# Performance work log

Hardware: AMD Instinct MI355X
Metric: run time of the kernel (lower is better)

The kernel has to match this reference:

```python
import jax, jax.numpy as jnp
import numpy as np

DIM = 768
HEADS = 12
DIM_HEAD = 64
INNER = HEADS * DIM_HEAD  # 768
EPS = 1e-5


def setup_inputs() -> dict:
    key = jax.random.key(0)
    ks = jax.random.split(key, 5)
    x = jax.random.normal(ks[0], (4, 2048, DIM), dtype=jnp.float32)
    ln_g = jnp.ones((DIM,), dtype=jnp.float32)
    ln_b = jnp.zeros((DIM,), dtype=jnp.float32)
    s1 = 1.0 / np.sqrt(DIM)
    W_qkv = jax.random.uniform(ks[1], (DIM, 3 * INNER), dtype=jnp.float32, minval=-s1, maxval=s1)
    b_qkv = jax.random.uniform(ks[2], (3 * INNER,), dtype=jnp.float32, minval=-s1, maxval=s1)
    s2 = 1.0 / np.sqrt(INNER)
    W_out = jax.random.uniform(ks[3], (INNER, DIM), dtype=jnp.float32, minval=-s2, maxval=s2)
    b_out = jax.random.uniform(ks[4], (DIM,), dtype=jnp.float32, minval=-s2, maxval=s2)
    return {"x": x, "ln_g": ln_g, "ln_b": ln_b, "W_qkv": W_qkv, "b_qkv": b_qkv, "W_out": W_out, "b_out": b_out}


def reference(x, ln_g, ln_b, W_qkv, b_qkv, W_out, b_out):
    b, n, _ = x.shape
    # pre-norm LayerNorm
    mu = jnp.mean(x, axis=-1, keepdims=True)
    var = jnp.mean(jnp.square(x - mu), axis=-1, keepdims=True)
    xn = (x - mu) * jax.lax.rsqrt(var + EPS) * ln_g + ln_b
    qkv = xn @ W_qkv + b_qkv  # [b, n, 3*inner]
    q, k, v = jnp.split(qkv, 3, axis=-1)
    def to_heads(t):
        return t.reshape(b, n, HEADS, DIM_HEAD).transpose(0, 2, 1, 3)  # b h n d
    q, k, v = map(to_heads, (q, k, v))
    q = q * (DIM_HEAD ** -0.5)
    sim = jnp.einsum('bhid,bhjd->bhij', q, k)
    attn = jax.nn.softmax(sim, axis=-1)  # dropout is identity (p=0.0)
    out = jnp.einsum('bhij,bhjd->bhid', attn, v)
    out = out.transpose(0, 2, 1, 3).reshape(b, n, INNER)
    return out @ W_out + b_out
```

## Files before the change

### kernel.cpp

```cpp
#include <hip/hip_runtime.h>
#include <cstdint>
#include <cstddef>


#define SEQ    2048
#define NBATCH 4
#define DMODEL 768
#define NHEADS 12
#define DHEAD  64
#define MROWS  (NBATCH * SEQ)
#define NQKV   (3 * DMODEL)
#define KT     64
#define NT     (SEQ / KT)

using f32x4  = __attribute__((ext_vector_type(4))) float;
using u16x8  = __attribute__((ext_vector_type(8))) unsigned short;
using s16x8  = __attribute__((ext_vector_type(8))) short;

__device__ __forceinline__ unsigned short f2bf(float f) {
  union { float f; unsigned int u; } x; x.f = f;
  unsigned int r = x.u + 0x7fffu + ((x.u >> 16) & 1u);
  return (unsigned short)(r >> 16);
}

#if defined(__has_builtin)
#if __has_builtin(__builtin_amdgcn_cvt_pk_bf16_f32)
#define HAVE_PK_BF16 1
#endif
#if __has_builtin(__builtin_amdgcn_exp2f)
#define HAVE_EXP2 1
#endif
#endif

__device__ __forceinline__ unsigned int pk_bf16(float a, float b) {
#ifdef HAVE_PK_BF16
  auto v = __builtin_amdgcn_cvt_pk_bf16_f32(a, b);
  union { decltype(v) v2; unsigned int u; } c; c.v2 = v; return c.u;
#else
  return (unsigned int)f2bf(a) | ((unsigned int)f2bf(b) << 16);
#endif
}

__device__ __forceinline__ float fexp2(float x) {
#ifdef HAVE_EXP2
  return __builtin_amdgcn_exp2f(x);
#else
  return exp2f(x);
#endif
}

__device__ __forceinline__ f32x4 mfma16(u16x8 a, u16x8 b, f32x4 c) {
  return __builtin_amdgcn_mfma_f32_16x16x32_bf16((s16x8)a, (s16x8)b, c, 0, 0, 0);
}

__device__ __forceinline__ void gl_lds16(const void* g, void* l) {
  __builtin_amdgcn_global_load_lds(
      (const __attribute__((address_space(1))) void*)g,
      (__attribute__((address_space(3))) void*)l, 16, 0, 0);
}

__global__ __launch_bounds__(256) void ln_kernel(
    const float* __restrict__ x, const float* __restrict__ g,
    const float* __restrict__ bb, unsigned short* __restrict__ xn) {
  __shared__ float red[8];
  const int row = blockIdx.x, t = threadIdx.x;
  const float* xr = x + (size_t)row * DMODEL;
  float v0 = xr[t], v1 = xr[t + 256], v2 = xr[t + 512];
  float s = v0 + v1 + v2;
#pragma unroll
  for (int o = 32; o; o >>= 1) s += __shfl_down(s, o);
  if ((t & 63) == 0) red[t >> 6] = s;
  __syncthreads();
  float mu = (red[0] + red[1] + red[2] + red[3]) * (1.0f / DMODEL);
  float d0 = v0 - mu, d1 = v1 - mu, d2 = v2 - mu;
  float q = d0 * d0 + d1 * d1 + d2 * d2;
#pragma unroll
  for (int o = 32; o; o >>= 1) q += __shfl_down(q, o);
  if ((t & 63) == 0) red[4 + (t >> 6)] = q;
  __syncthreads();
  float var = (red[4] + red[5] + red[6] + red[7]) * (1.0f / DMODEL);
  float rstd = rsqrtf(var + 1e-5f);
  size_t base = (size_t)row * DMODEL;
  xn[base + t]       = f2bf(d0 * rstd * g[t]       + bb[t]);
  xn[base + t + 256] = f2bf(d1 * rstd * g[t + 256] + bb[t + 256]);
  xn[base + t + 512] = f2bf(d2 * rstd * g[t + 512] + bb[t + 512]);
}

__global__ __launch_bounds__(256) void tconv_kernel(
    const float* __restrict__ W, unsigned short* __restrict__ Wt, int N) {
  __shared__ float tile[32][33];
  const int n0 = blockIdx.x * 32, k0 = blockIdx.y * 32;
  const int tx = threadIdx.x & 31, ty = threadIdx.x >> 5;
#pragma unroll
  for (int r = 0; r < 4; ++r)
    tile[ty + r * 8][tx] = W[(size_t)(k0 + ty + r * 8) * N + n0 + tx];
  __syncthreads();
#pragma unroll
  for (int r = 0; r < 4; ++r)
    Wt[(size_t)(n0 + ty + r * 8) * DMODEL + k0 + tx] = f2bf(tile[tx][ty + r * 8]);
}

__global__ __launch_bounds__(256, 2) void gemm_qk_kernel(
    const unsigned short* __restrict__ Wt, const unsigned short* __restrict__ xn,
    const float* __restrict__ bias, unsigned short* __restrict__ qb,
    unsigned short* __restrict__ kb) {
  __shared__ alignas(16) unsigned short As[128 * 64];
  __shared__ alignas(16) unsigned short Bs[128 * 64];
  const int t = threadIdx.x, wid = t >> 6, l = t & 63, quad = l >> 4, ll = l & 15;
  const int a0 = blockIdx.x * 128;
  const int b0 = blockIdx.y * 128;
  const int wa = (wid >> 1) * 64, wb = (wid & 1) * 64;
  const int srow = l >> 3, sblk = (l & 7) ^ srow;
  f32x4 acc[4][4] = {};
  for (int k0 = 0; k0 < DMODEL; k0 += 64) {
#pragma unroll
    for (int cc = 0; cc < 4; ++cc) {
      int call = wid * 4 + cc;
      int r = call * 8 + srow;
      gl_lds16(Wt + (size_t)(a0 + r) * DMODEL + k0 + sblk * 8, &As[call * 512]);
      gl_lds16(xn + (size_t)(b0 + r) * DMODEL + k0 + sblk * 8, &Bs[call * 512]);
    }
    __syncthreads();
#pragma unroll
    for (int ks = 0; ks < 2; ++ks) {
      u16x8 af[4], bf[4];
#pragma unroll
      for (int i = 0; i < 4; ++i) {
        int ra = wa + i * 16 + ll, rb = wb + i * 16 + ll;
        int blk = (ks * 4 + quad) ^ (ll & 7);
        af[i] = *(const u16x8*)&As[ra * 64 + blk * 8];
        bf[i] = *(const u16x8*)&Bs[rb * 64 + blk * 8];
      }
#pragma unroll
      for (int mi = 0; mi < 4; ++mi)
#pragma unroll
        for (int ni = 0; ni < 4; ++ni)
          acc[mi][ni] = mfma16(af[mi], bf[ni], acc[mi][ni]);
    }
    __syncthreads();
  }
  const bool isq = (a0 < DMODEL);
  unsigned short* dst = isq ? qb : kb;
  const float sc = isq ? 0.18033688f : 1.0f;
#pragma unroll
  for (int mi = 0; mi < 4; ++mi) {
    int row0 = a0 + wa + mi * 16 + quad * 4;
    float4 bv = *(const float4*)&bias[row0];
    int rr = isq ? row0 : row0 - DMODEL;
    int h = rr >> 6, d0 = rr & 63;
#pragma unroll
    for (int ni = 0; ni < 4; ++ni) {
      int seq = b0 + wb + ni * 16 + ll;
      int b = seq >> 11, i = seq & 2047;
      uint2 pk;
      pk.x = pk_bf16((acc[mi][ni][0] + bv.x) * sc, (acc[mi][ni][1] + bv.y) * sc);
      pk.y = pk_bf16((acc[mi][ni][2] + bv.z) * sc, (acc[mi][ni][3] + bv.w) * sc);
      *(uint2*)&dst[(size_t)((b * NHEADS + h) * SEQ + i) * DHEAD + d0] = pk;
    }
  }
}

__global__ __launch_bounds__(256, 2) void gemm_v_kernel(
    const unsigned short* __restrict__ A, const unsigned short* __restrict__ Bt,
    const float* __restrict__ bias, unsigned short* __restrict__ vt) {
  __shared__ alignas(16) unsigned short As[128 * 64];
  __shared__ alignas(16) unsigned short Bs[128 * 64];
  const int t = threadIdx.x, wid = t >> 6, l = t & 63, quad = l >> 4, ll = l & 15;
  const int m0 = blockIdx.x * 128;
  const int n0 = 2 * DMODEL + blockIdx.y * 128;
  const int wm = (wid >> 1) * 64, wn = (wid & 1) * 64;
  const int srow = l >> 3, sblk = (l & 7) ^ srow;
  f32x4 acc[4][4] = {};
  for (int k0 = 0; k0 < DMODEL; k0 += 64) {
#pragma unroll
    for (int cc = 0; cc < 4; ++cc) {
      int call = wid * 4 + cc;
      int r = call * 8 + srow;
      gl_lds16(A  + (size_t)(m0 + r) * DMODEL + k0 + sblk * 8, &As[call * 512]);
      gl_lds16(Bt + (size_t)(n0 + r) * DMODEL + k0 + sblk * 8, &Bs[call * 512]);
    }
    __syncthreads();
#pragma unroll
    for (int ks = 0; ks < 2; ++ks) {
      u16x8 af[4], bf[4];
#pragma unroll
      for (int i = 0; i < 4; ++i) {
        int ra = wm + i * 16 + ll, rb = wn + i * 16 + ll;
        int blk = (ks * 4 + quad) ^ (ll & 7);
        af[i] = *(const u16x8*)&As[ra * 64 + blk * 8];
        bf[i] = *(const u16x8*)&Bs[rb * 64 + blk * 8];
      }
#pragma unroll
      for (int mi = 0; mi < 4; ++mi)
#pragma unroll
        for (int ni = 0; ni < 4; ++ni)
          acc[mi][ni] = mfma16(af[mi], bf[ni], acc[mi][ni]);
    }
    __syncthreads();
  }
#pragma unroll
  for (int mi = 0; mi < 4; ++mi) {
    int gm = m0 + wm + mi * 16 + quad * 4;
    int b = gm >> 11, i0 = gm & 2047;
#pragma unroll
    for (int ni = 0; ni < 4; ++ni) {
      int gn = n0 + wn + ni * 16 + ll;
      float bv = bias[gn];
      int rem = gn - 2 * DMODEL;
      int h = rem >> 6, d = rem & 63;
      int bh = b * NHEADS + h;
      uint2 pk;
      pk.x = pk_bf16(acc[mi][ni][0] + bv, acc[mi][ni][1] + bv);
      pk.y = pk_bf16(acc[mi][ni][2] + bv, acc[mi][ni][3] + bv);
      *(uint2*)&vt[((size_t)bh * DHEAD + d) * SEQ + i0] = pk;
    }
  }
}

__global__ __launch_bounds__(256, 3) void attn_kernel(
    const unsigned short* __restrict__ qbuf, const unsigned short* __restrict__ kbuf,
    const unsigned short* __restrict__ vtg, unsigned short* __restrict__ ao) {
  __shared__ alignas(16) unsigned short stage[2][2][KT * DHEAD];
  __shared__ alignas(16) unsigned short Pws[4][32 * 72];
  const int t = threadIdx.x, wid = t >> 6, l = t & 63, quad = l >> 4, ll = l & 15;
  const int qt = blockIdx.x, bh = blockIdx.y;
  const unsigned short* qg  = qbuf + ((size_t)bh * SEQ + qt * 128) * DHEAD;
  const unsigned short* kg0 = kbuf + (size_t)bh * SEQ * DHEAD;
  const unsigned short* vt0 = vtg  + (size_t)bh * DHEAD * SEQ;
  const int srow = l >> 3;
  const int sblk = (l & 7) ^ srow;

  unsigned short* Qs = &stage[0][0][0];
#pragma unroll
  for (int cc = 0; cc < 4; ++cc) {
    int call = wid * 4 + cc;
    gl_lds16(qg + (call * 8 + srow) * 64 + sblk * 8, Qs + call * 512);
  }
  __syncthreads();
  u16x8 qf[2][2];
#pragma unroll
  for (int mi = 0; mi < 2; ++mi)
#pragma unroll
    for (int ks = 0; ks < 2; ++ks) {
      int r = wid * 32 + mi * 16 + ll;
      int blk = (ks * 4 + quad) ^ (ll & 7);
      qf[mi][ks] = *(const u16x8*)&Qs[r * 64 + blk * 8];
    }
  __syncthreads();

  auto stage_tile = [&](int buf, int kt2) {
    const unsigned short* kg = kg0 + (size_t)kt2 * KT * DHEAD;
#pragma unroll
    for (int c = 0; c < 2; ++c) {
      int call = wid * 2 + c;
      int r = call * 8 + srow;
      gl_lds16(kg + r * 64 + sblk * 8, &stage[buf][0][call * 512]);
      gl_lds16(vt0 + (size_t)r * SEQ + kt2 * KT + sblk * 8, &stage[buf][1][call * 512]);
    }
  };

  f32x4 oacc[2][4] = {};
  float lsum[2] = {0.f, 0.f};
  unsigned short* Pw = Pws[wid];

  stage_tile(0, 0);
  int buf = 0;
  for (int kt2 = 0; kt2 < NT; ++kt2) {
    __syncthreads();
    if (kt2 + 1 < NT) stage_tile(buf ^ 1, kt2 + 1);
    const unsigned short* Ks = &stage[buf][0][0];
    const unsigned short* Vs = &stage[buf][1][0];

    f32x4 st[2][4] = {};
#pragma unroll
    for (int ks = 0; ks < 2; ++ks)
#pragma unroll
      for (int ni = 0; ni < 4; ++ni) {
        int r = ni * 16 + ll;
        int blk = (ks * 4 + quad) ^ (ll & 7);
        u16x8 kf = *(const u16x8*)&Ks[r * 64 + blk * 8];
        st[0][ni] = mfma16(kf, qf[0][ks], st[0][ni]);
        st[1][ni] = mfma16(kf, qf[1][ks], st[1][ni]);
      }

#pragma unroll
    for (int mi = 0; mi < 2; ++mi)
#pragma unroll
      for (int ni = 0; ni < 4; ++ni) {
        float p0 = fexp2(st[mi][ni][0]);
        float p1 = fexp2(st[mi][ni][1]);
        float p2 = fexp2(st[mi][ni][2]);
        float p3 = fexp2(st[mi][ni][3]);
        lsum[mi] += (p0 + p1) + (p2 + p3);
        uint2 pk;
        pk.x = pk_bf16(p0, p1);
        pk.y = pk_bf16(p2, p3);
        *(uint2*)&Pw[(mi * 16 + ll) * 72 + ni * 16 + quad * 4] = pk;
      }
    asm volatile("s_waitcnt lgkmcnt(0)" ::: "memory");

#pragma unroll
    for (int ks = 0; ks < 2; ++ks) {
      u16x8 pf0 = *(const u16x8*)&Pw[(ll) * 72 + ks * 32 + quad * 8];
      u16x8 pf1 = *(const u16x8*)&Pw[(16 + ll) * 72 + ks * 32 + quad * 8];
#pragma unroll
      for (int di = 0; di < 4; ++di) {
        int r = di * 16 + ll;
        int blk = (ks * 4 + quad) ^ (ll & 7);
        u16x8 vf = *(const u16x8*)&Vs[r * 64 + blk * 8];
        oacc[0][di] = mfma16(pf0, vf, oacc[0][di]);
        oacc[1][di] = mfma16(pf1, vf, oacc[1][di]);
      }
    }
    buf ^= 1;
  }

  float lsF[2];
#pragma unroll
  for (int mi = 0; mi < 2; ++mi) {
    float ls = lsum[mi];
    ls += __shfl_xor(ls, 16);
    ls += __shfl_xor(ls, 32);
    lsF[mi] = ls;
  }

  const int b = bh / NHEADS, h = bh - b * NHEADS;
#pragma unroll
  for (int mi = 0; mi < 2; ++mi) {
#pragma unroll
    for (int r = 0; r < 4; ++r) {
      float inv = 1.0f / __shfl(lsF[mi], quad * 4 + r);
      int row = qt * 128 + wid * 32 + mi * 16 + quad * 4 + r;
      size_t base = ((size_t)(b * SEQ + row)) * DMODEL + h * DHEAD;
#pragma unroll
      for (int di = 0; di < 4; ++di)
        ao[base + di * 16 + ll] = f2bf(oacc[mi][di][r] * inv);
    }
  }
}

__global__ __launch_bounds__(256, 2) void gemm_out_kernel(
    const unsigned short* __restrict__ Wt, const unsigned short* __restrict__ ao,
    const float* __restrict__ bias, float* __restrict__ out) {
  __shared__ alignas(16) unsigned short As[128 * 64];
  __shared__ alignas(16) unsigned short Bs[128 * 64];
  const int t = threadIdx.x, wid = t >> 6, l = t & 63, quad = l >> 4, ll = l & 15;
  const int a0 = blockIdx.x * 128;
  const int b0 = blockIdx.y * 128;
  const int wa = (wid >> 1) * 64, wb = (wid & 1) * 64;
  const int srow = l >> 3, sblk = (l & 7) ^ srow;
  f32x4 acc[4][4] = {};
  for (int k0 = 0; k0 < DMODEL; k0 += 64) {
#pragma unroll
    for (int cc = 0; cc < 4; ++cc) {
      int call = wid * 4 + cc;
      int r = call * 8 + srow;
      gl_lds16(Wt + (size_t)(a0 + r) * DMODEL + k0 + sblk * 8, &As[call * 512]);
      gl_lds16(ao + (size_t)(b0 + r) * DMODEL + k0 + sblk * 8, &Bs[call * 512]);
    }
    __syncthreads();
#pragma unroll
    for (int ks = 0; ks < 2; ++ks) {
      u16x8 af[4], bf[4];
#pragma unroll
      for (int i = 0; i < 4; ++i) {
        int ra = wa + i * 16 + ll, rb = wb + i * 16 + ll;
        int blk = (ks * 4 + quad) ^ (ll & 7);
        af[i] = *(const u16x8*)&As[ra * 64 + blk * 8];
        bf[i] = *(const u16x8*)&Bs[rb * 64 + blk * 8];
      }
#pragma unroll
      for (int mi = 0; mi < 4; ++mi)
#pragma unroll
        for (int ni = 0; ni < 4; ++ni)
          acc[mi][ni] = mfma16(af[mi], bf[ni], acc[mi][ni]);
    }
    __syncthreads();
  }
#pragma unroll
  for (int mi = 0; mi < 4; ++mi) {
    int row0 = a0 + wa + mi * 16 + quad * 4;
    float4 bv = *(const float4*)&bias[row0];
#pragma unroll
    for (int ni = 0; ni < 4; ++ni) {
      int seq = b0 + wb + ni * 16 + ll;
      float4 o;
      o.x = acc[mi][ni][0] + bv.x;
      o.y = acc[mi][ni][1] + bv.y;
      o.z = acc[mi][ni][2] + bv.z;
      o.w = acc[mi][ni][3] + bv.w;
      *(float4*)&out[(size_t)seq * DMODEL + row0] = o;
    }
  }
}

extern "C" void kernel_launch(void* const* d_in, const int* in_sizes, int n_in,
                              void* d_out, int out_size, void* d_ws, size_t ws_size,
                              hipStream_t stream) {
  const float* x     = (const float*)d_in[0];
  const float* ln_g  = (const float*)d_in[1];
  const float* ln_b  = (const float*)d_in[2];
  const float* W_qkv = (const float*)d_in[3];
  const float* b_qkv = (const float*)d_in[4];
  const float* W_out = (const float*)d_in[5];
  const float* b_out = (const float*)d_in[6];
  float* out = (float*)d_out;

  char* ws = (char*)d_ws;
  unsigned short* xn    = (unsigned short*)(ws);
  unsigned short* wqkvt = (unsigned short*)(ws + 12582912);
  unsigned short* woutt = (unsigned short*)(ws + 16121856);
  unsigned short* qb    = (unsigned short*)(ws + 17301504);
  unsigned short* kb    = (unsigned short*)(ws + 29884416);
  unsigned short* vt    = (unsigned short*)(ws + 42467328);
  unsigned short* ao    = xn;

  ln_kernel<<<MROWS, 256, 0, stream>>>(x, ln_g, ln_b, xn);
  tconv_kernel<<<dim3(NQKV / 32, DMODEL / 32), 256, 0, stream>>>(W_qkv, wqkvt, NQKV);
  tconv_kernel<<<dim3(DMODEL / 32, DMODEL / 32), 256, 0, stream>>>(W_out, woutt, DMODEL);
  gemm_qk_kernel<<<dim3(12, 64), 256, 0, stream>>>(wqkvt, xn, b_qkv, qb, kb);
  gemm_v_kernel<<<dim3(64, 6), 256, 0, stream>>>(xn, wqkvt, b_qkv, vt);
  attn_kernel<<<dim3(SEQ / 128, NBATCH * NHEADS), 256, 0, stream>>>(qb, kb, vt, ao);
  gemm_out_kernel<<<dim3(6, 64), 256, 0, stream>>>(woutt, ao, b_out, out);
}
```

Measured before the change: 240.2 us.

## Pass softmax probabilities between lanes via shuffles and reorder attention grid

The attention kernel no longer writes the bf16 probability tile to per-wave shared memory and reads it back. It rebuilds the MFMA A-operand fragments directly from registers using cross-lane shuffles with a select on the upper quads. This removes the LDS round trip and the lgkmcnt wait, and frees shared memory that may allow more resident blocks, at the cost of many ds_bpermute-style shuffles. The grid is also swapped so batch-head is the fast dimension, which changes which blocks run concurrently and how K/V tiles hit in L2.

```diff
diff --git a/kernel.cpp b/kernel.cpp
--- a/kernel.cpp
+++ b/kernel.cpp
@@ -221,9 +221,8 @@
     const unsigned short* __restrict__ qbuf, const unsigned short* __restrict__ kbuf,
     const unsigned short* __restrict__ vtg, unsigned short* __restrict__ ao) {
   __shared__ alignas(16) unsigned short stage[2][2][KT * DHEAD];
-  __shared__ alignas(16) unsigned short Pws[4][32 * 72];
   const int t = threadIdx.x, wid = t >> 6, l = t & 63, quad = l >> 4, ll = l & 15;
-  const int qt = blockIdx.x, bh = blockIdx.y;
+  const int bh = blockIdx.x, qt = blockIdx.y;
   const unsigned short* qg  = qbuf + ((size_t)bh * SEQ + qt * 128) * DHEAD;
   const unsigned short* kg0 = kbuf + (size_t)bh * SEQ * DHEAD;
   const unsigned short* vt0 = vtg  + (size_t)bh * DHEAD * SEQ;
@@ -261,7 +260,7 @@
 
   f32x4 oacc[2][4] = {};
   float lsum[2] = {0.f, 0.f};
-  unsigned short* Pw = Pws[wid];
+  const bool hiq = (quad & 2) != 0;
 
   stage_tile(0, 0);
   int buf = 0;
@@ -283,6 +282,7 @@
         st[1][ni] = mfma16(kf, qf[1][ks], st[1][ni]);
       }
 
+    unsigned int pkv[2][4][2];
 #pragma unroll
     for (int mi = 0; mi < 2; ++mi)
 #pragma unroll
@@ -292,26 +292,36 @@
         float p2 = fexp2(st[mi][ni][2]);
         float p3 = fexp2(st[mi][ni][3]);
         lsum[mi] += (p0 + p1) + (p2 + p3);
-        uint2 pk;
-        pk.x = pk_bf16(p0, p1);
-        pk.y = pk_bf16(p2, p3);
-        *(uint2*)&Pw[(mi * 16 + ll) * 72 + ni * 16 + quad * 4] = pk;
-      }
-    asm volatile("s_waitcnt lgkmcnt(0)" ::: "memory");
-
-#pragma unroll
-    for (int ks = 0; ks < 2; ++ks) {
-      u16x8 pf0 = *(const u16x8*)&Pw[(ll) * 72 + ks * 32 + quad * 8];
-      u16x8 pf1 = *(const u16x8*)&Pw[(16 + ll) * 72 + ks * 32 + quad * 8];
+        pkv[mi][ni][0] = pk_bf16(p0, p1);
+        pkv[mi][ni][1] = pk_bf16(p2, p3);
+      }
+
+    u16x8 pfr[2][2];
+#pragma unroll
+    for (int mi = 0; mi < 2; ++mi)
+#pragma unroll
+      for (int ks = 0; ks < 2; ++ks) {
+        union { u16x8 v; unsigned int d[4]; } pf;
+#pragma unroll
+        for (int d = 0; d < 4; ++d) {
+          int src = (((2 * quad + (d >> 1)) & 3) << 4) | ll;
+          unsigned int lo = (unsigned int)__shfl((int)pkv[mi][ks * 2][d & 1], src, 64);
+          unsigned int hi = (unsigned int)__shfl((int)pkv[mi][ks * 2 + 1][d & 1], src, 64);
+          pf.d[d] = hiq ? hi : lo;
+        }
+        pfr[mi][ks] = pf.v;
+      }
+
+#pragma unroll
+    for (int ks = 0; ks < 2; ++ks)
 #pragma unroll
       for (int di = 0; di < 4; ++di) {
         int r = di * 16 + ll;
         int blk = (ks * 4 + quad) ^ (ll & 7);
         u16x8 vf = *(const u16x8*)&Vs[r * 64 + blk * 8];
-        oacc[0][di] = mfma16(pf0, vf, oacc[0][di]);
-        oacc[1][di] = mfma16(pf1, vf, oacc[1][di]);
-      }
-    }
+        oacc[0][di] = mfma16(pfr[0][ks], vf, oacc[0][di]);
+        oacc[1][di] = mfma16(pfr[1][ks], vf, oacc[1][di]);
+      }
     buf ^= 1;
   }
 
@@ -420,6 +430,6 @@
   tconv_kernel<<<dim3(DMODEL / 32, DMODEL / 32), 256, 0, stream>>>(W_out, woutt, DMODEL);
   gemm_qk_kernel<<<dim3(12, 64), 256, 0, stream>>>(wqkvt, xn, b_qkv, qb, kb);
   gemm_v_kernel<<<dim3(64, 6), 256, 0, stream>>>(xn, wqkvt, b_qkv, vt);
-  attn_kernel<<<dim3(SEQ / 128, NBATCH * NHEADS), 256, 0, stream>>>(qb, kb, vt, ao);
+  attn_kernel<<<dim3(NBATCH * NHEADS, SEQ / 128), 256, 0, stream>>>(qb, kb, vt, ao);
   gemm_out_kernel<<<dim3(6, 64), 256, 0, stream>>>(woutt, ao, b_out, out);
 }
```

Result: slower. 247.9 us (+3.2%).

## Use 2-wave attention blocks with 64 query rows per wave

Applied to the files above, without the earlier changes.

The attention kernel now runs 128 threads (2 waves) per 128-row query tile, so each wave handles 64 query rows and reuses each K and V fragment loaded from LDS across four MFMA row groups instead of two. K fragments are loaded once per tile and the QK product is computed per row group, which bounds live score registers. The grid is also swapped so consecutive blocks cover different heads at the same query tile. More accumulators per wave raise register pressure and there are fewer waves per block to hide latency.

```diff
diff --git a/kernel.cpp b/kernel.cpp
--- a/kernel.cpp
+++ b/kernel.cpp
@@ -217,13 +217,13 @@
   }
 }
 
-__global__ __launch_bounds__(256, 3) void attn_kernel(
+__global__ __launch_bounds__(128, 2) void attn_kernel(
     const unsigned short* __restrict__ qbuf, const unsigned short* __restrict__ kbuf,
     const unsigned short* __restrict__ vtg, unsigned short* __restrict__ ao) {
   __shared__ alignas(16) unsigned short stage[2][2][KT * DHEAD];
-  __shared__ alignas(16) unsigned short Pws[4][32 * 72];
+  __shared__ alignas(16) unsigned short Pws[2][64 * 72];
   const int t = threadIdx.x, wid = t >> 6, l = t & 63, quad = l >> 4, ll = l & 15;
-  const int qt = blockIdx.x, bh = blockIdx.y;
+  const int bh = blockIdx.x, qt = blockIdx.y;
   const unsigned short* qg  = qbuf + ((size_t)bh * SEQ + qt * 128) * DHEAD;
   const unsigned short* kg0 = kbuf + (size_t)bh * SEQ * DHEAD;
   const unsigned short* vt0 = vtg  + (size_t)bh * DHEAD * SEQ;
@@ -232,17 +232,17 @@
 
   unsigned short* Qs = &stage[0][0][0];
 #pragma unroll
-  for (int cc = 0; cc < 4; ++cc) {
-    int call = wid * 4 + cc;
+  for (int cc = 0; cc < 8; ++cc) {
+    int call = wid * 8 + cc;
     gl_lds16(qg + (call * 8 + srow) * 64 + sblk * 8, Qs + call * 512);
   }
   __syncthreads();
-  u16x8 qf[2][2];
-#pragma unroll
-  for (int mi = 0; mi < 2; ++mi)
+  u16x8 qf[4][2];
+#pragma unroll
+  for (int mi = 0; mi < 4; ++mi)
 #pragma unroll
     for (int ks = 0; ks < 2; ++ks) {
-      int r = wid * 32 + mi * 16 + ll;
+      int r = wid * 64 + mi * 16 + ll;
       int blk = (ks * 4 + quad) ^ (ll & 7);
       qf[mi][ks] = *(const u16x8*)&Qs[r * 64 + blk * 8];
     }
@@ -251,16 +251,16 @@
   auto stage_tile = [&](int buf, int kt2) {
     const unsigned short* kg = kg0 + (size_t)kt2 * KT * DHEAD;
 #pragma unroll
-    for (int c = 0; c < 2; ++c) {
-      int call = wid * 2 + c;
+    for (int c = 0; c < 4; ++c) {
+      int call = wid * 4 + c;
       int r = call * 8 + srow;
       gl_lds16(kg + r * 64 + sblk * 8, &stage[buf][0][call * 512]);
       gl_lds16(vt0 + (size_t)r * SEQ + kt2 * KT + sblk * 8, &stage[buf][1][call * 512]);
     }
   };
 
-  f32x4 oacc[2][4] = {};
-  float lsum[2] = {0.f, 0.f};
+  f32x4 oacc[4][4] = {};
+  float lsum[4] = {0.f, 0.f, 0.f, 0.f};
   unsigned short* Pw = Pws[wid];
 
   stage_tile(0, 0);
@@ -271,53 +271,62 @@
     const unsigned short* Ks = &stage[buf][0][0];
     const unsigned short* Vs = &stage[buf][1][0];
 
-    f32x4 st[2][4] = {};
+    u16x8 kf[2][4];
 #pragma unroll
     for (int ks = 0; ks < 2; ++ks)
 #pragma unroll
       for (int ni = 0; ni < 4; ++ni) {
         int r = ni * 16 + ll;
         int blk = (ks * 4 + quad) ^ (ll & 7);
-        u16x8 kf = *(const u16x8*)&Ks[r * 64 + blk * 8];
-        st[0][ni] = mfma16(kf, qf[0][ks], st[0][ni]);
-        st[1][ni] = mfma16(kf, qf[1][ks], st[1][ni]);
-      }
-
-#pragma unroll
-    for (int mi = 0; mi < 2; ++mi)
+        kf[ks][ni] = *(const u16x8*)&Ks[r * 64 + blk * 8];
+      }
+
+#pragma unroll
+    for (int mi = 0; mi < 4; ++mi) {
+      f32x4 st[4] = {};
+#pragma unroll
+      for (int ks = 0; ks < 2; ++ks)
+#pragma unroll
+        for (int ni = 0; ni < 4; ++ni)
+          st[ni] = mfma16(kf[ks][ni], qf[mi][ks], st[ni]);
 #pragma unroll
       for (int ni = 0; ni < 4; ++ni) {
-        float p0 = fexp2(st[mi][ni][0]);
-        float p1 = fexp2(st[mi][ni][1]);
-        float p2 = fexp2(st[mi][ni][2]);
-        float p3 = fexp2(st[mi][ni][3]);
+        float p0 = fexp2(st[ni][0]);
+        float p1 = fexp2(st[ni][1]);
+        float p2 = fexp2(st[ni][2]);
+        float p3 = fexp2(st[ni][3]);
         lsum[mi] += (p0 + p1) + (p2 + p3);
         uint2 pk;
         pk.x = pk_bf16(p0, p1);
         pk.y = pk_bf16(p2, p3);
         *(uint2*)&Pw[(mi * 16 + ll) * 72 + ni * 16 + quad * 4] = pk;
       }
+    }
     asm volatile("s_waitcnt lgkmcnt(0)" ::: "memory");
 
-#pragma unroll
-    for (int ks = 0; ks < 2; ++ks) {
-      u16x8 pf0 = *(const u16x8*)&Pw[(ll) * 72 + ks * 32 + quad * 8];
-      u16x8 pf1 = *(const u16x8*)&Pw[(16 + ll) * 72 + ks * 32 + quad * 8];
+    u16x8 pf[4][2];
+#pragma unroll
+    for (int mi = 0; mi < 4; ++mi)
+#pragma unroll
+      for (int ks = 0; ks < 2; ++ks)
+        pf[mi][ks] = *(const u16x8*)&Pw[(mi * 16 + ll) * 72 + ks * 32 + quad * 8];
+#pragma unroll
+    for (int ks = 0; ks < 2; ++ks)
 #pragma unroll
       for (int di = 0; di < 4; ++di) {
         int r = di * 16 + ll;
         int blk = (ks * 4 + quad) ^ (ll & 7);
         u16x8 vf = *(const u16x8*)&Vs[r * 64 + blk * 8];
-        oacc[0][di] = mfma16(pf0, vf, oacc[0][di]);
-        oacc[1][di] = mfma16(pf1, vf, oacc[1][di]);
-      }
-    }
+#pragma unroll
+        for (int mi = 0; mi < 4; ++mi)
+          oacc[mi][di] = mfma16(pf[mi][ks], vf, oacc[mi][di]);
+      }
     buf ^= 1;
   }
 
-  float lsF[2];
-#pragma unroll
-  for (int mi = 0; mi < 2; ++mi) {
+  float lsF[4];
+#pragma unroll
+  for (int mi = 0; mi < 4; ++mi) {
     float ls = lsum[mi];
     ls += __shfl_xor(ls, 16);
     ls += __shfl_xor(ls, 32);
@@ -326,11 +335,11 @@
 
   const int b = bh / NHEADS, h = bh - b * NHEADS;
 #pragma unroll
-  for (int mi = 0; mi < 2; ++mi) {
+  for (int mi = 0; mi < 4; ++mi) {
 #pragma unroll
     for (int r = 0; r < 4; ++r) {
       float inv = 1.0f / __shfl(lsF[mi], quad * 4 + r);
-      int row = qt * 128 + wid * 32 + mi * 16 + quad * 4 + r;
+      int row = qt * 128 + wid * 64 + mi * 16 + quad * 4 + r;
       size_t base = ((size_t)(b * SEQ + row)) * DMODEL + h * DHEAD;
 #pragma unroll
       for (int di = 0; di < 4; ++di)
@@ -420,6 +429,6 @@
   tconv_kernel<<<dim3(DMODEL / 32, DMODEL / 32), 256, 0, stream>>>(W_out, woutt, DMODEL);
   gemm_qk_kernel<<<dim3(12, 64), 256, 0, stream>>>(wqkvt, xn, b_qkv, qb, kb);
   gemm_v_kernel<<<dim3(64, 6), 256, 0, stream>>>(xn, wqkvt, b_qkv, vt);
-  attn_kernel<<<dim3(SEQ / 128, NBATCH * NHEADS), 256, 0, stream>>>(qb, kb, vt, ao);
+  attn_kernel<<<dim3(NBATCH * NHEADS, SEQ / 128), 128, 0, stream>>>(qb, kb, vt, ao);
   gemm_out_kernel<<<dim3(6, 64), 256, 0, stream>>>(woutt, ao, b_out, out);
 }
```

New measurement: 256.4 us. 6.7% more time.
